# Kernel optimization log

Measured on AMD Instinct MI355X. Metric: run time of the kernel, lower is better.

Reference implementation:

```python
import jax, jax.numpy as jnp
import numpy as np

N_NODES = 100000
Z_DIM = 64
N_EDGES = 1000000
H = 64

def setup_inputs() -> dict:
    key = jax.random.key(0)
    k1, k2, k3, k4 = jax.random.split(key, 4)
    z = jax.random.normal(k1, (N_NODES, Z_DIM), dtype=jnp.float32)
    edge = jax.random.randint(k2, (2, N_EDGES), 0, N_NODES, dtype=jnp.int64)
    # Linear params (stored as [in, out] for x @ W + b)
    W1 = jax.random.normal(k3, (2 * Z_DIM, H), dtype=jnp.float32) * (1.0 / np.sqrt(2 * Z_DIM))
    b1 = jnp.zeros((H,), dtype=jnp.float32)
    W2 = jax.random.normal(k4, (H, 1), dtype=jnp.float32) * (1.0 / np.sqrt(H))
    b2 = jnp.zeros((1,), dtype=jnp.float32)
    return {"z": z, "edge": edge, "W1": W1, "b1": b1, "W2": W2, "b2": b2}

def reference(z, edge, W1, b1, W2, b2):
    zi = z[edge[0]]                      # [E, z_dim] gather
    zj = z[edge[1]]                      # [E, z_dim] gather
    h = jnp.concatenate([zi, zj], axis=-1)  # [E, 2*z_dim]
    h = jax.nn.relu(h @ W1 + b1)         # [E, H]
    out = h @ W2 + b2                    # [E, 1]
    return out.squeeze(-1)               # [E]
```

## Files before the change

### kernel.cpp

```cpp
#include <hip/hip_runtime.h>
#include <hip/hip_bf16.h>

typedef unsigned short u16;
typedef unsigned int u32;
typedef __attribute__((ext_vector_type(8))) short bf16x8;
typedef __attribute__((ext_vector_type(16))) float f32x16;
typedef _Float16 h16x2 __attribute__((ext_vector_type(2)));

static __device__ __forceinline__ u16 f2bf(float f) {
    __hip_bfloat16 b = __float2bfloat16(f);
    return *(u16*)&b;
}

__global__ __launch_bounds__(256) void build_wfrag(
    const float* __restrict__ W1, u16* __restrict__ wtab)
{
    const int flat = blockIdx.x * 256 + threadIdx.x;
    if (flat >= 8192) return;
    const int j    = flat & 7;
    const int lane = (flat >> 3) & 63;
    const int ks   = (flat >> 9) & 3;
    const int ct   = flat >> 11;
    const int k = ks * 16 + (lane >> 5) * 8 + j;
    const int c = ct * 32 + (lane & 31);
    const float v = (c < 64) ? W1[(size_t)k * 64 + c]
                             : W1[(size_t)(64 + k) * 64 + (c - 64)];
    wtab[flat] = f2bf(v);
}

__global__ __launch_bounds__(256) void node_mfma(
    const float* __restrict__ z, const u16* __restrict__ wtab,
    const float* __restrict__ b1, u16* __restrict__ pq, int nNodes)
{
    const int lane   = threadIdx.x & 63;
    const int wave   = threadIdx.x >> 6;
    const int l31    = lane & 31;
    const int half   = lane >> 5;
    const int nodeBase = (blockIdx.x * 4 + wave) * 32;
    if (nodeBase >= nNodes) return;

    const bf16x8* wt = (const bf16x8*)wtab;
    bf16x8 Wf[4][4];
#pragma unroll
    for (int ct = 0; ct < 4; ++ct)
#pragma unroll
        for (int ks = 0; ks < 4; ++ks)
            Wf[ct][ks] = wt[(ct * 4 + ks) * 64 + lane];

    int zrowi = nodeBase + l31;
    if (zrowi > nNodes - 1) zrowi = nNodes - 1;
    const float* zrow = z + (size_t)zrowi * 64;
    bf16x8 Zf[4];
#pragma unroll
    for (int ks = 0; ks < 4; ++ks) {
        const float4 v0 = *(const float4*)(zrow + ks * 16 + half * 8);
        const float4 v1 = *(const float4*)(zrow + ks * 16 + half * 8 + 4);
        Zf[ks][0] = (short)f2bf(v0.x); Zf[ks][1] = (short)f2bf(v0.y);
        Zf[ks][2] = (short)f2bf(v0.z); Zf[ks][3] = (short)f2bf(v0.w);
        Zf[ks][4] = (short)f2bf(v1.x); Zf[ks][5] = (short)f2bf(v1.y);
        Zf[ks][6] = (short)f2bf(v1.z); Zf[ks][7] = (short)f2bf(v1.w);
    }

    f32x16 acc[4];
#pragma unroll
    for (int ct = 0; ct < 4; ++ct) acc[ct] = (f32x16)(0.0f);
#pragma unroll
    for (int ks = 0; ks < 4; ++ks)
#pragma unroll
        for (int ct = 0; ct < 4; ++ct)
            acc[ct] = __builtin_amdgcn_mfma_f32_32x32x16_bf16(
                Wf[ct][ks], Zf[ks], acc[ct], 0, 0, 0);

    const int node = nodeBase + l31;
    if (node < nNodes) {
        u16* prow = pq + (size_t)node * 128;
#pragma unroll
        for (int ct = 0; ct < 4; ++ct) {
#pragma unroll
            for (int g = 0; g < 4; ++g) {
                const int c0 = ct * 32 + 8 * g + 4 * half;
                float v0 = acc[ct][4 * g + 0];
                float v1 = acc[ct][4 * g + 1];
                float v2 = acc[ct][4 * g + 2];
                float v3 = acc[ct][4 * g + 3];
                if (ct < 2) {
                    v0 += b1[c0 + 0]; v1 += b1[c0 + 1];
                    v2 += b1[c0 + 2]; v3 += b1[c0 + 3];
                }
                uint2 st;
                st.x = __builtin_bit_cast(u32, __builtin_amdgcn_cvt_pkrtz(v0, v1));
                st.y = __builtin_bit_cast(u32, __builtin_amdgcn_cvt_pkrtz(v2, v3));
                *(uint2*)(prow + c0) = st;
            }
        }
    }
}

__global__ __launch_bounds__(256) void edge_mlp(
    const int* __restrict__ e0, const int* __restrict__ e1,
    const u16* __restrict__ pq, const float* __restrict__ W2,
    const float* __restrict__ b2, float* __restrict__ out, int E)
{
    const int gid = blockIdx.x * 256 + threadIdx.x;
    const int e   = gid >> 3;
    const int sub = gid & 7;
    if (e >= E) return;

    const int i = e0[e];
    const int j = e1[e];

    const uint4 p = ((const uint4*)(pq + (size_t)i * 128))[sub];
    const uint4 q = ((const uint4*)(pq + (size_t)j * 128 + 64))[sub];

    const float4 wa = ((const float4*)W2)[2 * sub];
    const float4 wb = ((const float4*)W2)[2 * sub + 1];

    const u32 pw[4] = {p.x, p.y, p.z, p.w};
    const u32 qw[4] = {q.x, q.y, q.z, q.w};

    h16x2 w2h[4];
    w2h[0] = (h16x2){(_Float16)wa.x, (_Float16)wa.y};
    w2h[1] = (h16x2){(_Float16)wa.z, (_Float16)wa.w};
    w2h[2] = (h16x2){(_Float16)wb.x, (_Float16)wb.y};
    w2h[3] = (h16x2){(_Float16)wb.z, (_Float16)wb.w};
    const h16x2 hzero = (h16x2){(_Float16)0.0f, (_Float16)0.0f};

    float sum = 0.0f;
#pragma unroll
    for (int c = 0; c < 4; ++c) {
        h16x2 pp = __builtin_bit_cast(h16x2, pw[c]);
        h16x2 qq = __builtin_bit_cast(h16x2, qw[c]);
        h16x2 a  = __builtin_elementwise_max(pp + qq, hzero);
#if __has_builtin(__builtin_amdgcn_fdot2)
        sum = __builtin_amdgcn_fdot2(a, w2h[c], sum, false);
#else
        sum = fmaf((float)a[0], (float)w2h[c][0],
              fmaf((float)a[1], (float)w2h[c][1], sum));
#endif
    }

    sum += __shfl_xor(sum, 1);
    sum += __shfl_xor(sum, 2);
    sum += __shfl_xor(sum, 4);

    if (sub == 0) out[e] = sum + b2[0];
}

extern "C" void kernel_launch(void* const* d_in, const int* in_sizes, int n_in,
                              void* d_out, int out_size, void* d_ws, size_t ws_size,
                              hipStream_t stream) {
    const float* z  = (const float*)d_in[0];
    const int*   eg = (const int*)d_in[1];
    const float* W1 = (const float*)d_in[2];
    const float* b1 = (const float*)d_in[3];
    const float* W2 = (const float*)d_in[4];
    const float* b2 = (const float*)d_in[5];
    float* out = (float*)d_out;

    const int nNodes = in_sizes[0] / 64;
    const int E      = in_sizes[1] / 2;

    u16* wtab = (u16*)d_ws;
    u16* pq   = (u16*)d_ws + 16384;

    build_wfrag<<<dim3(32), dim3(256), 0, stream>>>(W1, wtab);

    dim3 gA((nNodes + 127) / 128);
    node_mfma<<<gA, dim3(256), 0, stream>>>(z, wtab, b1, pq, nNodes);

    long long tB = (long long)E * 8;
    dim3 gB((unsigned)((tB + 255) / 256));
    edge_mlp<<<gB, dim3(256), 0, stream>>>(eg, eg + E, pq, W2, b2, out, E);
}
```

Before: 128.8 us.

## Bucket edges by source node and stage source rows in LDS

Replaces the direct per-edge gather kernel with a counting-sort pipeline. A histogram of source-node buckets (128 nodes each) is built, scanned, and used to scatter compact edge records into bucket order. A processing kernel then loads each bucket's 128 source rows into shared memory and reads only the destination rows from global memory. The aim is to halve random global gathers, at the cost of three extra launches, atomic-heavy scatter traffic, scattered output writes and a small grid with long serial loops per block.

```diff
diff --git a/kernel.cpp b/kernel.cpp
--- a/kernel.cpp
+++ b/kernel.cpp
@@ -7,15 +7,19 @@
 typedef __attribute__((ext_vector_type(16))) float f32x16;
 typedef _Float16 h16x2 __attribute__((ext_vector_type(2)));
 
+#define NBUCK  1024
+#define BSHIFT 7
+
 static __device__ __forceinline__ u16 f2bf(float f) {
     __hip_bfloat16 b = __float2bfloat16(f);
     return *(u16*)&b;
 }
 
 __global__ __launch_bounds__(256) void build_wfrag(
-    const float* __restrict__ W1, u16* __restrict__ wtab)
+    const float* __restrict__ W1, u16* __restrict__ wtab, u32* __restrict__ hist)
 {
     const int flat = blockIdx.x * 256 + threadIdx.x;
+    if (flat < NBUCK) hist[flat] = 0;
     if (flat >= 8192) return;
     const int j    = flat & 7;
     const int lane = (flat >> 3) & 63;
@@ -96,54 +100,113 @@
     }
 }
 
-__global__ __launch_bounds__(256) void edge_mlp(
+__global__ __launch_bounds__(256) void hist_k(
+    const int* __restrict__ e0, u32* __restrict__ hist, int E)
+{
+    __shared__ u32 lh[NBUCK];
+    for (int t = threadIdx.x; t < NBUCK; t += 256) lh[t] = 0;
+    __syncthreads();
+    for (int e = blockIdx.x * 256 + threadIdx.x; e < E; e += gridDim.x * 256)
+        atomicAdd(&lh[((u32)e0[e]) >> BSHIFT], 1);
+    __syncthreads();
+    for (int t = threadIdx.x; t < NBUCK; t += 256)
+        if (lh[t]) atomicAdd(&hist[t], lh[t]);
+}
+
+__global__ __launch_bounds__(1024) void scan_k(
+    const u32* __restrict__ hist, u32* __restrict__ base, u32* __restrict__ cursor)
+{
+    __shared__ u32 s[NBUCK];
+    const int t = threadIdx.x;
+    const u32 mine = hist[t];
+    s[t] = mine;
+    __syncthreads();
+    for (int off = 1; off < NBUCK; off <<= 1) {
+        u32 v = (t >= off) ? s[t - off] : 0;
+        __syncthreads();
+        s[t] += v;
+        __syncthreads();
+    }
+    const u32 ex = s[t] - mine;
+    base[t] = ex;
+    cursor[t] = ex;
+    if (t == NBUCK - 1) base[NBUCK] = s[t];
+}
+
+__global__ __launch_bounds__(256) void scatter_k(
     const int* __restrict__ e0, const int* __restrict__ e1,
+    u32* __restrict__ cursor, uint2* __restrict__ recs, int E)
+{
+    const int e = blockIdx.x * 256 + threadIdx.x;
+    if (e >= E) return;
+    const u32 i = (u32)e0[e];
+    const u32 j = (u32)e1[e];
+    const u32 pos = atomicAdd(&cursor[i >> BSHIFT], 1);
+    uint2 r; r.x = j; r.y = (u32)e | ((i & 127u) << 20);
+    recs[pos] = r;
+}
+
+__global__ __launch_bounds__(256) void process_k(
+    const uint2* __restrict__ recs, const u32* __restrict__ base,
     const u16* __restrict__ pq, const float* __restrict__ W2,
-    const float* __restrict__ b2, float* __restrict__ out, int E)
-{
-    const int gid = blockIdx.x * 256 + threadIdx.x;
-    const int e   = gid >> 3;
-    const int sub = gid & 7;
-    if (e >= E) return;
-
-    const int i = e0[e];
-    const int j = e1[e];
-
-    const uint4 p = ((const uint4*)(pq + (size_t)i * 128))[sub];
-    const uint4 q = ((const uint4*)(pq + (size_t)j * 128 + 64))[sub];
+    const float* __restrict__ b2, float* __restrict__ out, int nNodes)
+{
+    __shared__ u16 Plds[128 * 64];
+    const int b   = blockIdx.x;
+    const int nb0 = b << BSHIFT;
+    const int tid = threadIdx.x;
+
+    const int nrows = (nNodes - nb0 > 128) ? 128 : (nNodes - nb0);
+    for (int f = tid; f < nrows * 8; f += 256) {
+        const int r = f >> 3, c = f & 7;
+        ((uint4*)Plds)[r * 8 + c] =
+            ((const uint4*)(pq + (size_t)(nb0 + r) * 128))[c];
+    }
+    __syncthreads();
+
+    const int g   = tid >> 3;
+    const int sub = tid & 7;
 
     const float4 wa = ((const float4*)W2)[2 * sub];
     const float4 wb = ((const float4*)W2)[2 * sub + 1];
-
-    const u32 pw[4] = {p.x, p.y, p.z, p.w};
-    const u32 qw[4] = {q.x, q.y, q.z, q.w};
-
     h16x2 w2h[4];
     w2h[0] = (h16x2){(_Float16)wa.x, (_Float16)wa.y};
     w2h[1] = (h16x2){(_Float16)wa.z, (_Float16)wa.w};
     w2h[2] = (h16x2){(_Float16)wb.x, (_Float16)wb.y};
     w2h[3] = (h16x2){(_Float16)wb.z, (_Float16)wb.w};
     const h16x2 hzero = (h16x2){(_Float16)0.0f, (_Float16)0.0f};
-
-    float sum = 0.0f;
-#pragma unroll
-    for (int c = 0; c < 4; ++c) {
-        h16x2 pp = __builtin_bit_cast(h16x2, pw[c]);
-        h16x2 qq = __builtin_bit_cast(h16x2, qw[c]);
-        h16x2 a  = __builtin_elementwise_max(pp + qq, hzero);
+    const float bias = b2[0];
+
+    const u32 lo = base[b], hi = base[b + 1];
+    for (u32 s = lo + g; s < hi; s += 32) {
+        const uint2 r = recs[s];
+        const u32 j  = r.x;
+        const u32 e  = r.y & 0xFFFFFu;
+        const u32 il = r.y >> 20;
+
+        const uint4 p = ((const uint4*)&Plds[il * 64])[sub];
+        const uint4 q = ((const uint4*)(pq + (size_t)j * 128 + 64))[sub];
+
+        const u32 pw[4] = {p.x, p.y, p.z, p.w};
+        const u32 qw[4] = {q.x, q.y, q.z, q.w};
+        float sum = 0.0f;
+#pragma unroll
+        for (int c = 0; c < 4; ++c) {
+            h16x2 pp = __builtin_bit_cast(h16x2, pw[c]);
+            h16x2 qq = __builtin_bit_cast(h16x2, qw[c]);
+            h16x2 a  = __builtin_elementwise_max(pp + qq, hzero);
 #if __has_builtin(__builtin_amdgcn_fdot2)
-        sum = __builtin_amdgcn_fdot2(a, w2h[c], sum, false);
+            sum = __builtin_amdgcn_fdot2(a, w2h[c], sum, false);
 #else
-        sum = fmaf((float)a[0], (float)w2h[c][0],
-              fmaf((float)a[1], (float)w2h[c][1], sum));
+            sum = fmaf((float)a[0], (float)w2h[c][0],
+                  fmaf((float)a[1], (float)w2h[c][1], sum));
 #endif
-    }
-
-    sum += __shfl_xor(sum, 1);
-    sum += __shfl_xor(sum, 2);
-    sum += __shfl_xor(sum, 4);
-
-    if (sub == 0) out[e] = sum + b2[0];
+        }
+        sum += __shfl_xor(sum, 1);
+        sum += __shfl_xor(sum, 2);
+        sum += __shfl_xor(sum, 4);
+        if (sub == 0) out[e] = sum + bias;
+    }
 }
 
 extern "C" void kernel_launch(void* const* d_in, const int* in_sizes, int n_in,
@@ -160,15 +223,26 @@
     const int nNodes = in_sizes[0] / 64;
     const int E      = in_sizes[1] / 2;
 
-    u16* wtab = (u16*)d_ws;
-    u16* pq   = (u16*)d_ws + 16384;
-
-    build_wfrag<<<dim3(32), dim3(256), 0, stream>>>(W1, wtab);
+    char* w = (char*)d_ws;
+    u16*   wtab   = (u16*)w;
+    u16*   pq     = (u16*)(w + 16384);
+    char*  p2     = w + 16384 + (size_t)nNodes * 256;
+    u32*   hist   = (u32*)p2;
+    u32*   base   = (u32*)(p2 + 4352);
+    u32*   cursor = (u32*)(p2 + 8704);
+    uint2* recs   = (uint2*)(p2 + 13056);
+
+    build_wfrag<<<dim3(32), dim3(256), 0, stream>>>(W1, wtab, hist);
 
     dim3 gA((nNodes + 127) / 128);
     node_mfma<<<gA, dim3(256), 0, stream>>>(z, wtab, b1, pq, nNodes);
 
-    long long tB = (long long)E * 8;
-    dim3 gB((unsigned)((tB + 255) / 256));
-    edge_mlp<<<gB, dim3(256), 0, stream>>>(eg, eg + E, pq, W2, b2, out, E);
-}
+    hist_k<<<dim3(256), dim3(256), 0, stream>>>(eg, hist, E);
+    scan_k<<<dim3(1), dim3(1024), 0, stream>>>(hist, base, cursor);
+    scatter_k<<<dim3((E + 255) / 256), dim3(256), 0, stream>>>(
+        eg, eg + E, cursor, recs, E);
+
+    const int nbUsed = (nNodes + 127) >> BSHIFT;
+    process_k<<<dim3(nbUsed), dim3(256), 0, stream>>>(
+        recs, base, pq, W2, b2, out, nNodes);
+}
```

New measurement: 383.9 us. 198% more time.
